# Kernel tuning notes

Hardware: AMD Instinct MI355X
Metric: run time of the kernel (lower is better)

Reference implementation:

```python
import jax, jax.numpy as jnp
import numpy as np

N_NODES = 100000
N_EDGES = 1600000
N_REL = 2
IN_CH, HID_CH, OUT_CH = 128, 128, 64


def setup_inputs() -> dict:
    key = jax.random.key(0)
    ks = jax.random.split(key, 8)
    x = jax.random.normal(ks[0], (N_NODES, IN_CH), dtype=jnp.float32)
    edge_index = jax.random.randint(ks[1], (2, N_EDGES), 0, N_NODES, dtype=jnp.int64)
    edge_type = jax.random.randint(ks[2], (N_EDGES,), 0, N_REL, dtype=jnp.int64)
    s1 = 1.0 / np.sqrt(IN_CH)
    s2 = 1.0 / np.sqrt(HID_CH)
    W1_rel = jax.random.normal(ks[3], (N_REL, IN_CH, HID_CH), dtype=jnp.float32) * s1
    W1_root = jax.random.normal(ks[4], (IN_CH, HID_CH), dtype=jnp.float32) * s1
    b1 = jnp.zeros((HID_CH,), dtype=jnp.float32)
    W2_rel = jax.random.normal(ks[5], (N_REL, HID_CH, OUT_CH), dtype=jnp.float32) * s2
    W2_root = jax.random.normal(ks[6], (HID_CH, OUT_CH), dtype=jnp.float32) * s2
    b2 = jnp.zeros((OUT_CH,), dtype=jnp.float32)
    return {"x": x, "edge_index": edge_index, "edge_type": edge_type,
            "W1_rel": W1_rel, "W1_root": W1_root, "b1": b1,
            "W2_rel": W2_rel, "W2_root": W2_root, "b2": b2}


def rgcn_conv(x, edge_index, edge_type, W_rel, W_root, b):
    """Relational graph conv: root transform + per-relation gather/matmul/scatter-mean."""
    src, dst = edge_index[0], edge_index[1]
    N = x.shape[0]
    out = x @ W_root + b  # self/root term
    x_src = x[src]  # [E, in] gather once, reused across relations
    for r in range(W_rel.shape[0]):  # N_REL is small and fixed
        mask = (edge_type == r)
        msg = jnp.where(mask[:, None], x_src, 0.0) @ W_rel[r]  # [E, out]
        agg = jax.ops.segment_sum(msg, dst, num_segments=N)  # [N, out]
        cnt = jax.ops.segment_sum(mask.astype(x.dtype), dst, num_segments=N)
        out = out + agg / jnp.maximum(cnt, 1.0)[:, None]  # mean aggregation
    return out


def l2_normalize(x, eps=1e-12):
    nrm = jnp.sqrt(jnp.sum(x * x, axis=1, keepdims=True))
    return x / jnp.maximum(nrm, eps)


def reference(x, edge_index, edge_type, W1_rel, W1_root, b1, W2_rel, W2_root, b2):
    h = jax.nn.relu(rgcn_conv(x, edge_index, edge_type, W1_rel, W1_root, b1))
    out = rgcn_conv(h, edge_index, edge_type, W2_rel, W2_root, b2)
    return l2_normalize(out)
```

## Files before the change

### kernel.cpp

```cpp
#include <hip/hip_runtime.h>
#include <hip/hip_bf16.h>


typedef unsigned int uint;
typedef unsigned short ushort;
typedef __attribute__((ext_vector_type(8))) short short8;
typedef __attribute__((ext_vector_type(16))) float floatx16;

#define IN_CH  128
#define OUT_CH 64
#define SCAN_CHUNK 2048
#define EPB 8192
#define KPB 512
#define MAXBK 400

__device__ __forceinline__ ushort f2bf(float f) {
    uint u = __float_as_uint(f);
    u += 0x7FFF + ((u >> 16) & 1);
    return (ushort)(u >> 16);
}
__device__ __forceinline__ float bflo(uint u) { return __uint_as_float(u << 16); }
__device__ __forceinline__ float bfhi(uint u) { return __uint_as_float(u & 0xFFFF0000u); }


__global__ void k_count(const int* __restrict__ dst, const int* __restrict__ et,
                        int* __restrict__ cntblk, int E, int NBK, int NBLK) {
    __shared__ int cnt[MAXBK];
    int tid = threadIdx.x, blk = blockIdx.x;
    for (int b = tid; b < NBK; b += 256) cnt[b] = 0;
    __syncthreads();
    int base = blk * EPB;
#pragma unroll 4
    for (int i = 0; i < EPB / 256; i++) {
        int e = base + i * 256 + tid;
        if (e < E) {
            int key = 2 * dst[e] + et[e];
            atomicAdd(&cnt[key >> 9], 1);
        }
    }
    __syncthreads();
    for (int b = tid; b < NBK; b += 256) cntblk[b * NBLK + blk] = cnt[b];
}

__global__ void k_scan_a(const int* __restrict__ deg, int* __restrict__ offs,
                         int* __restrict__ bsums, int n) {
    __shared__ int sdata[256];
    int b = blockIdx.x, t = threadIdx.x;
    int base = b * SCAN_CHUNK + t * 8;
    int v[8];
    int sum = 0;
#pragma unroll
    for (int i = 0; i < 8; i++) {
        int idx = base + i;
        int x = (idx < n) ? deg[idx] : 0;
        v[i] = sum;
        sum += x;
    }
    sdata[t] = sum;
    __syncthreads();
    for (int ofs = 1; ofs < 256; ofs <<= 1) {
        int val = sdata[t];
        int add = (t >= ofs) ? sdata[t - ofs] : 0;
        __syncthreads();
        sdata[t] = val + add;
        __syncthreads();
    }
    int texcl = (t == 0) ? 0 : sdata[t - 1];
    if (t == 255) bsums[b] = sdata[255];
#pragma unroll
    for (int i = 0; i < 8; i++) {
        int idx = base + i;
        if (idx < n) offs[idx] = texcl + v[i];
    }
}

__global__ void k_scan_b(int* __restrict__ bsums, int* __restrict__ offs, int nb, int n) {
    if (blockIdx.x == 0 && threadIdx.x == 0) {
        int run = 0;
        for (int b = 0; b < nb; b++) {
            int t = bsums[b];
            bsums[b] = run;
            run += t;
        }
        offs[n] = run;
    }
}

__global__ void k_scan_c(int* __restrict__ offs, const int* __restrict__ bsums, int n) {
    int i = blockIdx.x * blockDim.x + threadIdx.x;
    if (i < n) offs[i] += bsums[i / SCAN_CHUNK];
}

__global__ void k_part(const int* __restrict__ src, const int* __restrict__ dst,
                       const int* __restrict__ et, const int* __restrict__ basebb,
                       uint* __restrict__ stage, int E, int NBK, int NBLK) {
    __shared__ int cnt[MAXBK];
    __shared__ int basel[MAXBK];
    int tid = threadIdx.x, blk = blockIdx.x;
    for (int b = tid; b < NBK; b += 256) {
        cnt[b] = 0;
        basel[b] = basebb[b * NBLK + blk];
    }
    __syncthreads();
    int base = blk * EPB;
#pragma unroll 4
    for (int i = 0; i < EPB / 256; i++) {
        int e = base + i * 256 + tid;
        if (e < E) {
            int s = src[e];
            int key = 2 * dst[e] + et[e];
            int bk = key >> 9;
            int r = atomicAdd(&cnt[bk], 1);
            stage[basel[bk] + r] = ((uint)(key & 511) << 23) | (uint)s;
        }
    }
}

__global__ void k_fine(const uint* __restrict__ stage, const int* __restrict__ basebb,
                       int* __restrict__ offs, int* __restrict__ esrc,
                       int E, int NBK, int NBLK) {
    __shared__ int kcnt[KPB];
    __shared__ int kcur[KPB];
    __shared__ int ssum[256];
    int tid = threadIdx.x, b = blockIdx.x;
    int start = basebb[b * NBLK];
    int endB = (b == NBK - 1) ? E : basebb[(b + 1) * NBLK];
    int size = endB - start;

    kcnt[tid] = 0;
    kcnt[tid + 256] = 0;
    __syncthreads();
    for (int i = tid; i < size; i += 256)
        atomicAdd(&kcnt[stage[start + i] >> 23], 1);
    __syncthreads();
    int v0 = kcnt[2 * tid], v1 = kcnt[2 * tid + 1];
    ssum[tid] = v0 + v1;
    __syncthreads();
    for (int ofs = 1; ofs < 256; ofs <<= 1) {
        int val = ssum[tid];
        int add = (tid >= ofs) ? ssum[tid - ofs] : 0;
        __syncthreads();
        ssum[tid] = val + add;
        __syncthreads();
    }
    int texcl = (tid == 0) ? 0 : ssum[tid - 1];
    kcur[2 * tid] = texcl;
    kcur[2 * tid + 1] = texcl + v0;
    offs[(b << 9) + 2 * tid] = start + texcl + v0;
    offs[(b << 9) + 2 * tid + 1] = start + texcl + v0 + v1;
    __syncthreads();
    for (int i = tid; i < size; i += 256) {
        uint p = stage[start + i];
        int r = atomicAdd(&kcur[p >> 23], 1);
        esrc[start + r] = (int)(p & 0x7FFFFFu);
    }
}


__global__ void k_cvt(const float* __restrict__ x, uint4* __restrict__ xb, int n8) {
    int i = blockIdx.x * 256 + threadIdx.x;
    if (i >= n8) return;
    const float4 f0 = ((const float4*)x)[(size_t)i * 2];
    const float4 f1 = ((const float4*)x)[(size_t)i * 2 + 1];
    uint4 o;
    o.x = (uint)f2bf(f0.x) | ((uint)f2bf(f0.y) << 16);
    o.y = (uint)f2bf(f0.z) | ((uint)f2bf(f0.w) << 16);
    o.z = (uint)f2bf(f1.x) | ((uint)f2bf(f1.y) << 16);
    o.w = (uint)f2bf(f1.z) | ((uint)f2bf(f1.w) << 16);
    xb[i] = o;
}


__device__ __forceinline__ uint4 pack8(const ushort* o) {
    uint4 v;
    v.x = (uint)o[0] | ((uint)o[1] << 16);
    v.y = (uint)o[2] | ((uint)o[3] << 16);
    v.z = (uint)o[4] | ((uint)o[5] << 16);
    v.w = (uint)o[6] | ((uint)o[7] << 16);
    return v;
}

__global__ void k_prep(const float* __restrict__ W1root, const float* __restrict__ W1rel,
                       const float* __restrict__ W2root, const float* __restrict__ W2rel,
                       uint4* __restrict__ Bpk1, uint4* __restrict__ Bpk2) {
    int idx = blockIdx.x * 256 + threadIdx.x;
    if (idx >= 10240) return;
    ushort o[8];
    if (idx < 6144) {
        int id = idx;
        int ct = id >> 11;
        int c = id & 2047;
        int gn = c >> 9, s = (c >> 6) & 7, h = (c >> 5) & 1, n = c & 31;
        int k0 = s * 16 + h * 8;
        int col = gn * 32 + n;
        const float* W = (ct == 0) ? W1root : (W1rel + (size_t)(ct - 1) * 16384);
#pragma unroll
        for (int j = 0; j < 8; j++) o[j] = f2bf(W[(k0 + j) * 128 + col]);
        Bpk1[id] = pack8(o);
    } else {
        int id = idx - 6144;
        int ct = id >> 11;
        int c = id & 2047;
        int gn = c >> 9, s = (c >> 6) & 7, h = (c >> 5) & 1, n = c & 31;
        int k0 = s * 16 + h * 8;
        int colg = ct * 128 + gn * 32 + n;
#pragma unroll
        for (int j = 0; j < 8; j++) {
            float f = 0.f;
            if (colg < 64)       f = W2root[(k0 + j) * 64 + colg];
            else if (colg < 128) f = W2rel[(k0 + j) * 64 + (colg - 64)];
            else if (colg < 192) f = W2rel[8192 + (k0 + j) * 64 + (colg - 128)];
            o[j] = f2bf(f);
        }
        Bpk2[id] = pack8(o);
    }
}


__global__ __launch_bounds__(256)
void k_agg(const int* __restrict__ offs, const int* __restrict__ esrc,
           const uint* __restrict__ xb, uint2* __restrict__ S, int N) {
    int wid = (int)((blockIdx.x * 256L + threadIdx.x) >> 6);
    int lane = threadIdx.x & 63;
    if (wid >= N) return;
    int sub = lane >> 5, cl = lane & 31;
    const uint2* F = (const uint2*)xb;

    int beg0 = (wid == 0) ? 0 : offs[2 * wid - 1];
    int end0 = offs[2 * wid], end1 = offs[2 * wid + 1];

    uint2 o = make_uint2(0, 0);
#pragma unroll
    for (int r = 0; r < 2; r++) {
        int beg = r ? end0 : beg0;
        int end = r ? end1 : end0;
        float a0 = 0.f, a1 = 0.f, a2 = 0.f, a3 = 0.f;
        for (int c0 = beg; c0 < end; c0 += 64) {
            int myid = (c0 + lane < end) ? esrc[c0 + lane] : N;
            int m = min(64, end - c0);
            for (int eb = 0; eb < m; eb += 8) {
                uint2 v[4];
#pragma unroll
                for (int j = 0; j < 4; j++) {
                    int id = __shfl(myid, eb + 2 * j + sub, 64);
                    v[j] = F[(size_t)id * 32 + cl];
                }
#pragma unroll
                for (int j = 0; j < 4; j++) {
                    a0 += bflo(v[j].x); a1 += bfhi(v[j].x);
                    a2 += bflo(v[j].y); a3 += bfhi(v[j].y);
                }
            }
        }
        a0 += __shfl_xor(a0, 32, 64);
        a1 += __shfl_xor(a1, 32, 64);
        a2 += __shfl_xor(a2, 32, 64);
        a3 += __shfl_xor(a3, 32, 64);
        if (sub == r) {
            float inv = (end > beg) ? 1.0f / (float)(end - beg) : 0.f;
            o.x = (uint)f2bf(a0 * inv) | ((uint)f2bf(a1 * inv) << 16);
            o.y = (uint)f2bf(a2 * inv) | ((uint)f2bf(a3 * inv) << 16);
        }
    }
    S[(size_t)wid * 64 + lane] = o;
}


__global__ __launch_bounds__(256)
void k_gemm1(const ushort* __restrict__ xb, const ushort* __restrict__ S1,
             const ushort* __restrict__ Bpk, const float* __restrict__ b1,
             ushort* __restrict__ h, int N) {
    __shared__ ushort SH[32768];
    ushort* Alds = SH;
    ushort* Blds = SH + 16384;

    const int tid = threadIdx.x;
    const int lane = tid & 63;
    const int w = tid >> 6;
    const int wm = w >> 1, wn = w & 1;
    const int rowBase = blockIdx.x * 128;

    floatx16 acc[2][2] = {};

#pragma unroll
    for (int seg = 0; seg < 3; seg++) {
        const ushort* Ap = (seg == 0) ? xb : S1;
        const int stride = (seg == 0) ? 128 : 256;
        const int aoff = (seg == 2) ? 128 : 0;
        const uint4* Bsrc = (const uint4*)Bpk + seg * 2048;
#pragma unroll
        for (int i = 0; i < 8; i++) {
            int c = tid + i * 256;
            int m = c & 31, hh = (c >> 5) & 1, s = (c >> 6) & 7, g = c >> 9;
            int row = rowBase + g * 32 + m;
            if (row >= N) row = N - 1;
            int kc = s * 2 + hh;
            ((uint4*)Alds)[c] = *(const uint4*)(Ap + (size_t)row * stride + aoff + kc * 8);
            ((uint4*)Blds)[c] = Bsrc[c];
        }
        __syncthreads();
#pragma unroll
        for (int s = 0; s < 8; s++) {
            short8 a0 = *(const short8*)&Alds[(((wm * 2 + 0) * 8 + s) * 64 + lane) * 8];
            short8 a1 = *(const short8*)&Alds[(((wm * 2 + 1) * 8 + s) * 64 + lane) * 8];
            short8 b0 = *(const short8*)&Blds[(((wn * 2 + 0) * 8 + s) * 64 + lane) * 8];
            short8 b1f = *(const short8*)&Blds[(((wn * 2 + 1) * 8 + s) * 64 + lane) * 8];
            acc[0][0] = __builtin_amdgcn_mfma_f32_32x32x16_bf16(a0, b0, acc[0][0], 0, 0, 0);
            acc[0][1] = __builtin_amdgcn_mfma_f32_32x32x16_bf16(a0, b1f, acc[0][1], 0, 0, 0);
            acc[1][0] = __builtin_amdgcn_mfma_f32_32x32x16_bf16(a1, b0, acc[1][0], 0, 0, 0);
            acc[1][1] = __builtin_amdgcn_mfma_f32_32x32x16_bf16(a1, b1f, acc[1][1], 0, 0, 0);
        }
        __syncthreads();
    }

    ushort* Clds = SH;
    const int qr = 4 * (lane >> 5);
    const int cl = lane & 31;
    float bb[2];
#pragma unroll
    for (int nt = 0; nt < 2; nt++) bb[nt] = b1[wn * 64 + nt * 32 + cl];
#pragma unroll
    for (int mt = 0; mt < 2; mt++)
#pragma unroll
        for (int nt = 0; nt < 2; nt++) {
#pragma unroll
            for (int reg = 0; reg < 16; reg++) {
                int rl = (reg & 3) + 8 * (reg >> 2) + qr;
                float v = fmaxf(acc[mt][nt][reg] + bb[nt], 0.f);
                Clds[(wm * 64 + mt * 32 + rl) * 136 + wn * 64 + nt * 32 + cl] = f2bf(v);
            }
        }
    __syncthreads();

    int r = tid >> 1, half = tid & 1;
    int grow = rowBase + r;
    if (grow < N) {
#pragma unroll
        for (int k = 0; k < 8; k++) {
            int c0 = half * 64 + k * 8;
            uint4 v = *(const uint4*)&Clds[r * 136 + c0];
            *(uint4*)(h + (size_t)grow * 128 + c0) = v;
        }
    }
}


__global__ __launch_bounds__(256)
void k_gemmT(const ushort* __restrict__ A, const ushort* __restrict__ Bpk,
             ushort* __restrict__ Out, int N, int Ld) {
    __shared__ ushort SH[32768];
    ushort* Alds = SH;
    ushort* Blds = SH + 16384;

    const int tid = threadIdx.x;
    const int lane = tid & 63;
    const int w = tid >> 6;
    const int wm = w >> 1, wn = w & 1;
    const int rowBase = blockIdx.x * 128;
    const int ct = blockIdx.y;
    const int colBase = ct * 128;

    const uint4* Bsrc = (const uint4*)Bpk + (size_t)ct * 2048;
#pragma unroll
    for (int i = 0; i < 8; i++) {
        int c = tid + i * 256;
        ((uint4*)Blds)[c] = Bsrc[c];
    }
#pragma unroll
    for (int i = 0; i < 8; i++) {
        int c = tid + i * 256;
        int m = c & 31, h = (c >> 5) & 1, s = (c >> 6) & 7, g = c >> 9;
        int row = rowBase + g * 32 + m;
        if (row >= N) row = N - 1;
        int kc = s * 2 + h;
        ((uint4*)Alds)[c] = *(const uint4*)(A + (size_t)row * 128 + kc * 8);
    }
    __syncthreads();

    floatx16 acc[2][2] = {};
#pragma unroll
    for (int s = 0; s < 8; s++) {
        short8 a0 = *(const short8*)&Alds[(((wm * 2 + 0) * 8 + s) * 64 + lane) * 8];
        short8 a1 = *(const short8*)&Alds[(((wm * 2 + 1) * 8 + s) * 64 + lane) * 8];
        short8 b0 = *(const short8*)&Blds[(((wn * 2 + 0) * 8 + s) * 64 + lane) * 8];
        short8 b1 = *(const short8*)&Blds[(((wn * 2 + 1) * 8 + s) * 64 + lane) * 8];
        acc[0][0] = __builtin_amdgcn_mfma_f32_32x32x16_bf16(a0, b0, acc[0][0], 0, 0, 0);
        acc[0][1] = __builtin_amdgcn_mfma_f32_32x32x16_bf16(a0, b1, acc[0][1], 0, 0, 0);
        acc[1][0] = __builtin_amdgcn_mfma_f32_32x32x16_bf16(a1, b0, acc[1][0], 0, 0, 0);
        acc[1][1] = __builtin_amdgcn_mfma_f32_32x32x16_bf16(a1, b1, acc[1][1], 0, 0, 0);
    }
    __syncthreads();

    ushort* Clds = SH;
    const int qr = 4 * (lane >> 5);
    const int cl = lane & 31;
#pragma unroll
    for (int mt = 0; mt < 2; mt++)
#pragma unroll
        for (int nt = 0; nt < 2; nt++) {
#pragma unroll
            for (int reg = 0; reg < 16; reg++) {
                int rl = (reg & 3) + 8 * (reg >> 2) + qr;
                Clds[(wm * 64 + mt * 32 + rl) * 136 + wn * 64 + nt * 32 + cl] =
                    f2bf(acc[mt][nt][reg]);
            }
        }
    __syncthreads();

    int r = tid >> 1, half = tid & 1;
    int grow = rowBase + r;
    if (grow < N) {
#pragma unroll
        for (int k = 0; k < 8; k++) {
            int c0 = half * 64 + k * 8;
            int col = colBase + c0;
            if (col < Ld) {
                uint4 v = *(const uint4*)&Clds[r * 136 + c0];
                *(uint4*)(Out + (size_t)grow * Ld + col) = v;
            }
        }
    }
}


__global__ __launch_bounds__(256)
void k_final(const ushort* __restrict__ T2, const float* __restrict__ b2,
             const int* __restrict__ offs, const int* __restrict__ esrc,
             float* __restrict__ out, int N) {
    int wid = (int)((blockIdx.x * 256L + threadIdx.x) >> 6);
    int lane = threadIdx.x & 63;
    if (wid >= N) return;
    int q = lane >> 4, c = lane & 15;
    const uint2* Tb = (const uint2*)T2;

    int beg0 = (wid == 0) ? 0 : offs[2 * wid - 1];
    int end0 = offs[2 * wid], end1 = offs[2 * wid + 1];

    float t0 = 0.f, t1 = 0.f, t2 = 0.f, t3 = 0.f;
#pragma unroll
    for (int r = 0; r < 2; r++) {
        int beg = r ? end0 : beg0;
        int end = r ? end1 : end0;
        if (end > beg) {
            float a0 = 0.f, a1 = 0.f, a2 = 0.f, a3 = 0.f;
            const uint2* Y = Tb + 16 + 16 * r + c;
            for (int c0 = beg; c0 < end; c0 += 64) {
                int myid = (c0 + lane < end) ? esrc[c0 + lane] : N;
                int m = min(64, end - c0);
                for (int eb = 0; eb < m; eb += 8) {
                    uint2 v[2];
#pragma unroll
                    for (int j = 0; j < 2; j++) {
                        int id = __shfl(myid, eb + 4 * j + q, 64);
                        v[j] = Y[(size_t)id * 48];
                    }
#pragma unroll
                    for (int j = 0; j < 2; j++) {
                        a0 += bflo(v[j].x); a1 += bfhi(v[j].x);
                        a2 += bflo(v[j].y); a3 += bfhi(v[j].y);
                    }
                }
            }
            float inv = 1.0f / (float)(end - beg);
            t0 += a0 * inv; t1 += a1 * inv; t2 += a2 * inv; t3 += a3 * inv;
        }
    }
#pragma unroll
    for (int d = 16; d <= 32; d <<= 1) {
        t0 += __shfl_xor(t0, d, 64);
        t1 += __shfl_xor(t1, d, 64);
        t2 += __shfl_xor(t2, d, 64);
        t3 += __shfl_xor(t3, d, 64);
    }
    uint2 ru = Tb[(size_t)wid * 48 + c];
    float4 bb = *(const float4*)(b2 + 4 * c);
    float v0 = bflo(ru.x) + bb.x + t0;
    float v1 = bfhi(ru.x) + bb.y + t1;
    float v2 = bflo(ru.y) + bb.z + t2;
    float v3 = bfhi(ru.y) + bb.w + t3;
    float sq = v0 * v0 + v1 * v1 + v2 * v2 + v3 * v3;
#pragma unroll
    for (int d = 1; d <= 8; d <<= 1) sq += __shfl_xor(sq, d, 64);
    float rn = 1.0f / fmaxf(sqrtf(sq), 1e-12f);
    if (lane < 16) {
        float4 o = {v0 * rn, v1 * rn, v2 * rn, v3 * rn};
        *(float4*)(out + (size_t)wid * 64 + 4 * c) = o;
    }
}


extern "C" void kernel_launch(void* const* d_in, const int* in_sizes, int n_in,
                              void* d_out, int out_size, void* d_ws, size_t ws_size,
                              hipStream_t stream) {
    const float* x      = (const float*)d_in[0];
    const int*   ei     = (const int*)d_in[1];
    const int*   etype  = (const int*)d_in[2];
    const float* W1rel  = (const float*)d_in[3];
    const float* W1root = (const float*)d_in[4];
    const float* b1     = (const float*)d_in[5];
    const float* W2rel  = (const float*)d_in[6];
    const float* W2root = (const float*)d_in[7];
    const float* b2     = (const float*)d_in[8];
    float* out = (float*)d_out;

    const int N = in_sizes[0] / IN_CH;
    const int E = in_sizes[2];
    const int NKEY = 2 * N;
    const int NBK  = (NKEY + KPB - 1) / KPB;
    const int NBLK = (E + EPB - 1) / EPB;
    const int NSC  = NBK * NBLK;

    const int* src = ei;
    const int* dst = ei + E;

    char* base = (char*)d_ws;
    size_t off = 0;
    auto carve = [&](size_t bytes) -> void* {
        void* p = base + off;
        off = (off + bytes + 511) & ~(size_t)511;
        return p;
    };
    ushort* xb    = (ushort*)carve((size_t)(N + 1) * 128 * sizeof(ushort));
    ushort* hA    = (ushort*)carve((size_t)N * 128 * sizeof(ushort));
    ushort* S1    = (ushort*)carve((size_t)N * 256 * sizeof(ushort));
    ushort* t2    = (ushort*)carve((size_t)(N + 1) * 192 * sizeof(ushort));
    int*    esrc  = (int*)carve((size_t)E * sizeof(int));
    uint*   stage = (uint*)carve((size_t)E * sizeof(uint));
    int*    offs  = (int*)carve((size_t)NBK * KPB * sizeof(int));
    int*    cntblk= (int*)carve((size_t)NSC * sizeof(int));
    int*    basebb= (int*)carve((size_t)(NSC + 1) * sizeof(int));
    int     NB    = (NSC + SCAN_CHUNK - 1) / SCAN_CHUNK;
    int*    bsums = (int*)carve((size_t)NB * sizeof(int));
    uint4*  Bpk1  = (uint4*)carve(6144 * sizeof(uint4));
    uint4*  Bpk2  = (uint4*)carve(4096 * sizeof(uint4));
    (void)ws_size; (void)n_in; (void)out_size;

    hipMemsetAsync(xb + (size_t)N * 128, 0, 128 * sizeof(ushort), stream);
    hipMemsetAsync(t2 + (size_t)N * 192, 0, 192 * sizeof(ushort), stream);

    k_count<<<NBLK, 256, 0, stream>>>(dst, etype, cntblk, E, NBK, NBLK);
    k_scan_a<<<NB, 256, 0, stream>>>(cntblk, basebb, bsums, NSC);
    k_scan_b<<<1, 64, 0, stream>>>(bsums, basebb, NB, NSC);
    k_scan_c<<<(NSC + 255) / 256, 256, 0, stream>>>(basebb, bsums, NSC);
    k_part<<<NBLK, 256, 0, stream>>>(src, dst, etype, basebb, stage, E, NBK, NBLK);
    k_fine<<<NBK, 256, 0, stream>>>(stage, basebb, offs, esrc, E, NBK, NBLK);

    int n8 = N * 16;
    k_cvt<<<(n8 + 255) / 256, 256, 0, stream>>>(x, (uint4*)xb, n8);
    k_prep<<<40, 256, 0, stream>>>(W1root, W1rel, W2root, W2rel, Bpk1, Bpk2);

    int rowTiles = (N + 127) / 128;
    int nodeBlocks = (int)(((long long)N * 64 + 255) / 256);

    k_agg<<<nodeBlocks, 256, 0, stream>>>(offs, esrc, (const uint*)xb, (uint2*)S1, N);
    k_gemm1<<<rowTiles, 256, 0, stream>>>(xb, S1, (const ushort*)Bpk1, b1, hA, N);

    k_gemmT<<<dim3(rowTiles, 2), 256, 0, stream>>>(hA, (const ushort*)Bpk2, t2, N, 192);
    k_final<<<nodeBlocks, 256, 0, stream>>>(t2, b2, offs, esrc, out, N);
}
```

Before: 372.8 us.

## Use half-wave per node with 16-byte gathers in aggregation kernels

The mean-aggregation and final gather kernels now assign 32 lanes per node instead of a full 64-lane wavefront, and each lane gathers a 16-byte uint4 row slice instead of 8 bytes. Accumulation uses packed float2 vectors and the reductions shrink to match the half-wave width. The single-thread block-sum scan is replaced by a wavefront shuffle scan when there are at most 64 blocks. The aim is fewer, wider memory requests per edge and twice the nodes per wavefront, at the cost of more registers per lane and lane divergence within a wave when neighbouring nodes have different degrees.

```diff
diff --git a/kernel.cpp b/kernel.cpp
--- a/kernel.cpp
+++ b/kernel.cpp
@@ -6,6 +6,7 @@
 typedef unsigned short ushort;
 typedef __attribute__((ext_vector_type(8))) short short8;
 typedef __attribute__((ext_vector_type(16))) float floatx16;
+typedef __attribute__((ext_vector_type(2))) float f32x2;
 
 #define IN_CH  128
 #define OUT_CH 64
@@ -75,12 +76,23 @@
 }
 
 __global__ void k_scan_b(int* __restrict__ bsums, int* __restrict__ offs, int nb, int n) {
-    if (blockIdx.x == 0 && threadIdx.x == 0) {
+    int t = threadIdx.x;
+    if (nb <= 64) {
+        int v = (t < nb) ? bsums[t] : 0;
+        int s = v;
+#pragma unroll
+        for (int d = 1; d < 64; d <<= 1) {
+            int u = __shfl_up(s, d, 64);
+            if (t >= d) s += u;
+        }
+        if (t < nb) bsums[t] = s - v;
+        if (t == 63) offs[n] = s;
+    } else if (t == 0) {
         int run = 0;
         for (int b = 0; b < nb; b++) {
-            int t = bsums[b];
+            int x = bsums[b];
             bsums[b] = run;
-            run += t;
+            run += x;
         }
         offs[n] = run;
     }
@@ -219,50 +231,49 @@
 
 __global__ __launch_bounds__(256)
 void k_agg(const int* __restrict__ offs, const int* __restrict__ esrc,
-           const uint* __restrict__ xb, uint2* __restrict__ S, int N) {
-    int wid = (int)((blockIdx.x * 256L + threadIdx.x) >> 6);
-    int lane = threadIdx.x & 63;
+           const uint4* __restrict__ xb4, uint4* __restrict__ S4, int N) {
+    int wid = (int)((blockIdx.x * 256L + threadIdx.x) >> 5);
+    int l = threadIdx.x & 31;
     if (wid >= N) return;
-    int sub = lane >> 5, cl = lane & 31;
-    const uint2* F = (const uint2*)xb;
+    int q = l >> 4, c = l & 15;
 
     int beg0 = (wid == 0) ? 0 : offs[2 * wid - 1];
     int end0 = offs[2 * wid], end1 = offs[2 * wid + 1];
 
-    uint2 o = make_uint2(0, 0);
+    uint4 o = make_uint4(0, 0, 0, 0);
 #pragma unroll
     for (int r = 0; r < 2; r++) {
         int beg = r ? end0 : beg0;
         int end = r ? end1 : end0;
-        float a0 = 0.f, a1 = 0.f, a2 = 0.f, a3 = 0.f;
-        for (int c0 = beg; c0 < end; c0 += 64) {
-            int myid = (c0 + lane < end) ? esrc[c0 + lane] : N;
-            int m = min(64, end - c0);
-            for (int eb = 0; eb < m; eb += 8) {
-                uint2 v[4];
-#pragma unroll
-                for (int j = 0; j < 4; j++) {
-                    int id = __shfl(myid, eb + 2 * j + sub, 64);
-                    v[j] = F[(size_t)id * 32 + cl];
-                }
-#pragma unroll
-                for (int j = 0; j < 4; j++) {
-                    a0 += bflo(v[j].x); a1 += bfhi(v[j].x);
-                    a2 += bflo(v[j].y); a3 += bfhi(v[j].y);
+        f32x2 a0 = {0.f, 0.f}, a1 = {0.f, 0.f}, a2 = {0.f, 0.f}, a3 = {0.f, 0.f};
+        for (int c0 = beg; c0 < end; c0 += 32) {
+            int myid = (c0 + l < end) ? esrc[c0 + l] : N;
+            int m = min(32, end - c0);
+            for (int eb = 0; eb < m; eb += 4) {
+#pragma unroll
+                for (int j = 0; j < 2; j++) {
+                    int id = __shfl(myid, eb + 2 * j + q, 32);
+                    uint4 v = xb4[(uint)id * 16u + (uint)c];
+                    a0 += (f32x2){bflo(v.x), bfhi(v.x)};
+                    a1 += (f32x2){bflo(v.y), bfhi(v.y)};
+                    a2 += (f32x2){bflo(v.z), bfhi(v.z)};
+                    a3 += (f32x2){bflo(v.w), bfhi(v.w)};
                 }
             }
         }
-        a0 += __shfl_xor(a0, 32, 64);
-        a1 += __shfl_xor(a1, 32, 64);
-        a2 += __shfl_xor(a2, 32, 64);
-        a3 += __shfl_xor(a3, 32, 64);
-        if (sub == r) {
+        a0.x += __shfl_xor(a0.x, 16, 32); a0.y += __shfl_xor(a0.y, 16, 32);
+        a1.x += __shfl_xor(a1.x, 16, 32); a1.y += __shfl_xor(a1.y, 16, 32);
+        a2.x += __shfl_xor(a2.x, 16, 32); a2.y += __shfl_xor(a2.y, 16, 32);
+        a3.x += __shfl_xor(a3.x, 16, 32); a3.y += __shfl_xor(a3.y, 16, 32);
+        if (q == r) {
             float inv = (end > beg) ? 1.0f / (float)(end - beg) : 0.f;
-            o.x = (uint)f2bf(a0 * inv) | ((uint)f2bf(a1 * inv) << 16);
-            o.y = (uint)f2bf(a2 * inv) | ((uint)f2bf(a3 * inv) << 16);
-        }
-    }
-    S[(size_t)wid * 64 + lane] = o;
+            o.x = (uint)f2bf(a0.x * inv) | ((uint)f2bf(a0.y * inv) << 16);
+            o.y = (uint)f2bf(a1.x * inv) | ((uint)f2bf(a1.y * inv) << 16);
+            o.z = (uint)f2bf(a2.x * inv) | ((uint)f2bf(a2.y * inv) << 16);
+            o.w = (uint)f2bf(a3.x * inv) | ((uint)f2bf(a3.y * inv) << 16);
+        }
+    }
+    S4[(size_t)wid * 32 + q * 16 + c] = o;
 }
 
 
@@ -427,64 +438,70 @@
 void k_final(const ushort* __restrict__ T2, const float* __restrict__ b2,
              const int* __restrict__ offs, const int* __restrict__ esrc,
              float* __restrict__ out, int N) {
-    int wid = (int)((blockIdx.x * 256L + threadIdx.x) >> 6);
-    int lane = threadIdx.x & 63;
+    int wid = (int)((blockIdx.x * 256L + threadIdx.x) >> 5);
+    int l = threadIdx.x & 31;
     if (wid >= N) return;
-    int q = lane >> 4, c = lane & 15;
-    const uint2* Tb = (const uint2*)T2;
+    int q = l >> 3, c = l & 7;
+    const uint4* Tb = (const uint4*)T2;
 
     int beg0 = (wid == 0) ? 0 : offs[2 * wid - 1];
     int end0 = offs[2 * wid], end1 = offs[2 * wid + 1];
 
-    float t0 = 0.f, t1 = 0.f, t2 = 0.f, t3 = 0.f;
+    f32x2 t0 = {0.f, 0.f}, t1 = {0.f, 0.f}, t2v = {0.f, 0.f}, t3v = {0.f, 0.f};
 #pragma unroll
     for (int r = 0; r < 2; r++) {
         int beg = r ? end0 : beg0;
         int end = r ? end1 : end0;
         if (end > beg) {
-            float a0 = 0.f, a1 = 0.f, a2 = 0.f, a3 = 0.f;
-            const uint2* Y = Tb + 16 + 16 * r + c;
-            for (int c0 = beg; c0 < end; c0 += 64) {
-                int myid = (c0 + lane < end) ? esrc[c0 + lane] : N;
-                int m = min(64, end - c0);
+            f32x2 a0 = {0.f, 0.f}, a1 = {0.f, 0.f}, a2 = {0.f, 0.f}, a3 = {0.f, 0.f};
+            uint bc = 8u + 8u * (uint)r + (uint)c;
+            for (int c0 = beg; c0 < end; c0 += 32) {
+                int myid = (c0 + l < end) ? esrc[c0 + l] : N;
+                int m = min(32, end - c0);
                 for (int eb = 0; eb < m; eb += 8) {
-                    uint2 v[2];
 #pragma unroll
                     for (int j = 0; j < 2; j++) {
-                        int id = __shfl(myid, eb + 4 * j + q, 64);
-                        v[j] = Y[(size_t)id * 48];
-                    }
-#pragma unroll
-                    for (int j = 0; j < 2; j++) {
-                        a0 += bflo(v[j].x); a1 += bfhi(v[j].x);
-                        a2 += bflo(v[j].y); a3 += bfhi(v[j].y);
+                        int id = __shfl(myid, eb + 4 * j + q, 32);
+                        uint4 v = Tb[(uint)id * 24u + bc];
+                        a0 += (f32x2){bflo(v.x), bfhi(v.x)};
+                        a1 += (f32x2){bflo(v.y), bfhi(v.y)};
+                        a2 += (f32x2){bflo(v.z), bfhi(v.z)};
+                        a3 += (f32x2){bflo(v.w), bfhi(v.w)};
                     }
                 }
             }
             float inv = 1.0f / (float)(end - beg);
-            t0 += a0 * inv; t1 += a1 * inv; t2 += a2 * inv; t3 += a3 * inv;
-        }
-    }
-#pragma unroll
-    for (int d = 16; d <= 32; d <<= 1) {
-        t0 += __shfl_xor(t0, d, 64);
-        t1 += __shfl_xor(t1, d, 64);
-        t2 += __shfl_xor(t2, d, 64);
-        t3 += __shfl_xor(t3, d, 64);
-    }
-    uint2 ru = Tb[(size_t)wid * 48 + c];
-    float4 bb = *(const float4*)(b2 + 4 * c);
-    float v0 = bflo(ru.x) + bb.x + t0;
-    float v1 = bfhi(ru.x) + bb.y + t1;
-    float v2 = bflo(ru.y) + bb.z + t2;
-    float v3 = bfhi(ru.y) + bb.w + t3;
-    float sq = v0 * v0 + v1 * v1 + v2 * v2 + v3 * v3;
-#pragma unroll
-    for (int d = 1; d <= 8; d <<= 1) sq += __shfl_xor(sq, d, 64);
+            t0 += a0 * inv; t1 += a1 * inv; t2v += a2 * inv; t3v += a3 * inv;
+        }
+    }
+#pragma unroll
+    for (int d = 8; d <= 16; d <<= 1) {
+        t0.x += __shfl_xor(t0.x, d, 32); t0.y += __shfl_xor(t0.y, d, 32);
+        t1.x += __shfl_xor(t1.x, d, 32); t1.y += __shfl_xor(t1.y, d, 32);
+        t2v.x += __shfl_xor(t2v.x, d, 32); t2v.y += __shfl_xor(t2v.y, d, 32);
+        t3v.x += __shfl_xor(t3v.x, d, 32); t3v.y += __shfl_xor(t3v.y, d, 32);
+    }
+    uint4 ru = Tb[(uint)wid * 24u + (uint)c];
+    float4 bbA = *(const float4*)(b2 + 8 * c);
+    float4 bbB = *(const float4*)(b2 + 8 * c + 4);
+    float v0 = bflo(ru.x) + bbA.x + t0.x;
+    float v1 = bfhi(ru.x) + bbA.y + t0.y;
+    float v2 = bflo(ru.y) + bbA.z + t1.x;
+    float v3 = bfhi(ru.y) + bbA.w + t1.y;
+    float v4 = bflo(ru.z) + bbB.x + t2v.x;
+    float v5 = bfhi(ru.z) + bbB.y + t2v.y;
+    float v6 = bflo(ru.w) + bbB.z + t3v.x;
+    float v7 = bfhi(ru.w) + bbB.w + t3v.y;
+    float sq = v0 * v0 + v1 * v1 + v2 * v2 + v3 * v3
+             + v4 * v4 + v5 * v5 + v6 * v6 + v7 * v7;
+#pragma unroll
+    for (int d = 1; d <= 4; d <<= 1) sq += __shfl_xor(sq, d, 32);
     float rn = 1.0f / fmaxf(sqrtf(sq), 1e-12f);
-    if (lane < 16) {
-        float4 o = {v0 * rn, v1 * rn, v2 * rn, v3 * rn};
-        *(float4*)(out + (size_t)wid * 64 + 4 * c) = o;
+    if (l < 8) {
+        float4 oA = {v0 * rn, v1 * rn, v2 * rn, v3 * rn};
+        float4 oB = {v4 * rn, v5 * rn, v6 * rn, v7 * rn};
+        *(float4*)(out + (size_t)wid * 64 + 8 * c) = oA;
+        *(float4*)(out + (size_t)wid * 64 + 8 * c + 4) = oB;
     }
 }
 
@@ -550,9 +567,9 @@
     k_prep<<<40, 256, 0, stream>>>(W1root, W1rel, W2root, W2rel, Bpk1, Bpk2);
 
     int rowTiles = (N + 127) / 128;
-    int nodeBlocks = (int)(((long long)N * 64 + 255) / 256);
-
-    k_agg<<<nodeBlocks, 256, 0, stream>>>(offs, esrc, (const uint*)xb, (uint2*)S1, N);
+    int nodeBlocks = (N + 7) / 8;
+
+    k_agg<<<nodeBlocks, 256, 0, stream>>>(offs, esrc, (const uint4*)xb, (uint4*)S1, N);
     k_gemm1<<<rowTiles, 256, 0, stream>>>(xb, S1, (const ushort*)Bpk1, b1, hA, N);
 
     k_gemmT<<<dim3(rowTiles, 2), 256, 0, stream>>>(hA, (const ushort*)Bpk2, t2, N, 192);
```

After: 354.0 us. -5.0%, faster.
